# Kernel optimization log

Hardware: AMD Instinct MI355X
Metric: run time of the kernel (lower is better)

Reference implementation:

```python
import jax, jax.numpy as jnp
import numpy as np

N = 50000      # nodes
E = 400000     # edges
F_IN = 128     # num_features
EMB = 64       # embedding_size
H1, H2, H3 = 4, 2, 1
G = 256        # number of graphs in batch
NEG_SLOPE = 0.2  # GATv2Conv default


def setup_inputs() -> dict:
    key = jax.random.key(0)
    ks = jax.random.split(key, 20)
    s = 0.1  # keep attention logits in a sane range
    return {
        "x": jax.random.normal(ks[0], (N, F_IN), dtype=jnp.float32),
        "edge_index": jax.random.randint(ks[1], (2, E), 0, N),
        "batch_index": jnp.sort(jax.random.randint(ks[2], (N,), 0, G)),
        "w1_l": jax.random.normal(ks[3], (H1 * EMB, F_IN), dtype=jnp.float32) * s,
        "w1_r": jax.random.normal(ks[4], (H1 * EMB, F_IN), dtype=jnp.float32) * s,
        "att1": jax.random.normal(ks[5], (H1, EMB), dtype=jnp.float32) * s,
        "b1": jax.random.normal(ks[6], (H1 * EMB,), dtype=jnp.float32) * s,
        "w2_l": jax.random.normal(ks[7], (H2 * EMB, H1 * EMB), dtype=jnp.float32) * s,
        "w2_r": jax.random.normal(ks[8], (H2 * EMB, H1 * EMB), dtype=jnp.float32) * s,
        "att2": jax.random.normal(ks[9], (H2, EMB), dtype=jnp.float32) * s,
        "b2": jax.random.normal(ks[10], (H2 * EMB,), dtype=jnp.float32) * s,
        "w3_l": jax.random.normal(ks[11], (H3 * EMB, H2 * EMB), dtype=jnp.float32) * s,
        "w3_r": jax.random.normal(ks[12], (H3 * EMB, H2 * EMB), dtype=jnp.float32) * s,
        "att3": jax.random.normal(ks[13], (H3, EMB), dtype=jnp.float32) * s,
        "b3": jax.random.normal(ks[14], (H3 * EMB,), dtype=jnp.float32) * s,
        "out_w": jax.random.normal(ks[15], (2, 2 * EMB), dtype=jnp.float32) * s,
        "out_b": jax.random.normal(ks[16], (2,), dtype=jnp.float32) * s,
    }


def gatv2_conv(x, src, dst, w_l, w_r, att, bias, heads):
    """PyG GATv2Conv (concat=True, add_self_loops already applied to src/dst)."""
    n = x.shape[0]
    d = att.shape[1]
    xl = (x @ w_l.T).reshape(n, heads, d)   # source transform
    xr = (x @ w_r.T).reshape(n, heads, d)   # target transform
    # per-edge attention logits: e_ij = att . leaky_relu(xl[j] + xr[i])
    z = jax.nn.leaky_relu(xl[src] + xr[dst], NEG_SLOPE)      # [E', H, D]
    e = jnp.einsum("ehd,hd->eh", z, att)                      # [E', H]
    # segment softmax over incoming edges of each target node
    m = jax.ops.segment_max(e, dst, num_segments=n)           # [N, H]
    p = jnp.exp(e - m[dst])
    ssum = jax.ops.segment_sum(p, dst, num_segments=n)        # [N, H]
    alpha = p / (ssum[dst] + 1e-16)
    out = jax.ops.segment_sum(alpha[:, :, None] * xl[src], dst, num_segments=n)
    return out.reshape(n, heads * d) + bias


def reference(x, edge_index, batch_index,
              w1_l, w1_r, att1, b1,
              w2_l, w2_r, att2, b2,
              w3_l, w3_r, att3, b3,
              out_w, out_b):
    n = x.shape[0]
    loop = jnp.arange(n, dtype=edge_index.dtype)
    src = jnp.concatenate([edge_index[0], loop])  # add self loops (PyG default)
    dst = jnp.concatenate([edge_index[1], loop])

    h = gatv2_conv(x, src, dst, w1_l, w1_r, att1, b1, H1)
    h = jax.nn.leaky_relu(h)  # slope 0.01 (F.leaky_relu default)
    h = gatv2_conv(h, src, dst, w2_l, w2_r, att2, b2, H2)
    h = jax.nn.leaky_relu(h)
    h = gatv2_conv(h, src, dst, w3_l, w3_r, att3, b3, H3)
    h = jax.nn.leaky_relu(h)

    # global max / mean pooling per graph
    gmax = jax.ops.segment_max(h, batch_index, num_segments=G)
    gsum = jax.ops.segment_sum(h, batch_index, num_segments=G)
    cnt = jax.ops.segment_sum(jnp.ones((n, 1), h.dtype), batch_index, num_segments=G)
    gmean = gsum / jnp.maximum(cnt, 1.0)
    hidden = jnp.concatenate([gmax, gmean], axis=1)           # [G, 2*EMB]
    out = hidden @ out_w.T + out_b                            # [G, 2]
    return (out, hidden)
```

## Files before the change

### kernel.cpp

```cpp
#include <hip/hip_runtime.h>
#include <hip/hip_bf16.h>
#include <cfloat>
#include <cstdint>


typedef __attribute__((ext_vector_type(8))) short bf16x8;
typedef __attribute__((ext_vector_type(4))) float f32x4;
typedef __attribute__((ext_vector_type(2))) float v2f;
typedef __attribute__((ext_vector_type(4))) unsigned short us4;
typedef __attribute__((ext_vector_type(2))) unsigned short us2;

#define L2E 1.4426950408889634f

__device__ __forceinline__ float bf2f(unsigned short u) {
    return __uint_as_float((unsigned)u << 16);
}
__device__ __forceinline__ unsigned short f2bf(float f) {
    unsigned u = __float_as_uint(f);
    u += 0x7FFFu + ((u >> 16) & 1u);
    return (unsigned short)(u >> 16);
}
__device__ __forceinline__ v2f unpack2(unsigned d) {
    v2f r;
    r.x = __uint_as_float(d << 16);
    r.y = __uint_as_float(d & 0xffff0000u);
    return r;
}
__device__ __forceinline__ unsigned pack2(float a, float b) {
    return (unsigned)f2bf(a) | ((unsigned)f2bf(b) << 16);
}

template<int CTRL>
__device__ __forceinline__ float dpp_add_f(float x) {
    int xi = __float_as_int(x);
    int yi = __builtin_amdgcn_update_dpp(xi, xi, CTRL, 0xF, 0xF, false);
    return x + __int_as_float(yi);
}
template<int PAT>
__device__ __forceinline__ float swz_add_f(float x) {
    int yi = __builtin_amdgcn_ds_swizzle(__float_as_int(x), PAT);
    return x + __int_as_float(yi);
}
template<int GS>
__device__ __forceinline__ float group_sum(float p) {
    p = dpp_add_f<0x121>(p);
    p = dpp_add_f<0x122>(p);
    p = dpp_add_f<0x124>(p);
    p = dpp_add_f<0x128>(p);
    if constexpr (GS >= 32) p = swz_add_f<0x401F>(p);
    if constexpr (GS >= 64) p += __shfl_xor(p, 32, 64);
    return p;
}

__global__ void init_k(int* __restrict__ deg, float* __restrict__ gsum,
                       float* __restrict__ gcnt, unsigned* __restrict__ gmaxu,
                       int N, int G)
{
    int i = blockIdx.x * blockDim.x + threadIdx.x;
    int stride = gridDim.x * blockDim.x;
    for (int k = i; k < N; k += stride) deg[k] = 0;
    for (int k = i; k < G * 64; k += stride) { gsum[k] = 0.f; gmaxu[k] = 0x00800000u; }
    for (int k = i; k < G; k += stride) gcnt[k] = 0.f;
}

__global__ void prep_k(const float* __restrict__ x, unsigned short* __restrict__ xb, int nx,
                       const float* p0, const float* p1, const float* p2,
                       const float* p3, const float* p4, const float* p5,
                       unsigned short* d0, unsigned short* d1, unsigned short* d2,
                       unsigned short* d3, unsigned short* d4, unsigned short* d5,
                       int s01, int s23, int s45,
                       const int* __restrict__ dste, int E, int N, int* __restrict__ deg)
{
    const int tid = blockIdx.x * blockDim.x + threadIdx.x;
    const int stride = gridDim.x * blockDim.x;

    for (int i = tid; i < nx / 4; i += stride) {
        int idx = i * 4;
        float4 v = *(const float4*)(x + idx);
        uint2 o = { pack2(v.x, v.y), pack2(v.z, v.w) };
        *(uint2*)(xb + idx) = o;
    }
    const int wtot4 = (2 * s01 + 2 * s23 + 2 * s45) / 4;
    const int t0 = 2 * s01, t1 = t0 + 2 * s23;
    for (int i = tid; i < wtot4; i += stride) {
        int e = i * 4;
        const float* s; unsigned short* d; int off;
        if (e < t0)      { int j = e;      s = (j < s01) ? p0 : p1; d = (j < s01) ? d0 : d1; off = j % s01; }
        else if (e < t1) { int j = e - t0; s = (j < s23) ? p2 : p3; d = (j < s23) ? d2 : d3; off = j % s23; }
        else             { int j = e - t1; s = (j < s45) ? p4 : p5; d = (j < s45) ? d4 : d5; off = j % s45; }
        float4 v = *(const float4*)(s + off);
        uint2 o = { pack2(v.x, v.y), pack2(v.z, v.w) };
        *(uint2*)(d + off) = o;
    }
    for (int e = tid; e < E + N; e += stride) {
        int i = (e < E) ? dste[e] : (e - E);
        atomicAdd(&deg[i], 1);
    }
}

template<int NT, int KT>
__global__ __launch_bounds__(256) void gemm_mfma(
    const __hip_bfloat16* __restrict__ A,
    const __hip_bfloat16* __restrict__ Wl, const __hip_bfloat16* __restrict__ Wr,
    __hip_bfloat16* __restrict__ Cl, __hip_bfloat16* __restrict__ Cr,
    int M, int Nout)
{
    constexpr int K = KT * 32;
    constexpr int LSTR = NT * 16 + 8;
    __shared__ unsigned short lds_c[4][32 * LSTR];
    const int wave = threadIdx.x >> 6, lane = threadIdx.x & 63;
    const int m0 = (blockIdx.x * 4 + wave) * 32;
    if (m0 >= M) return;
    const __hip_bfloat16* W = blockIdx.y ? Wr : Wl;
    __hip_bfloat16* C = blockIdx.y ? Cr : Cl;
    const int nbase = blockIdx.z * NT * 16;
    const int r16  = lane & 15;
    const int quad = lane >> 4;
    const int kq = quad * 8;

    f32x4 acc[2][NT];
    #pragma unroll
    for (int mt = 0; mt < 2; ++mt)
        #pragma unroll
        for (int n = 0; n < NT; ++n) acc[mt][n] = (f32x4){0.f, 0.f, 0.f, 0.f};

    const __hip_bfloat16* Arow[2];
    #pragma unroll
    for (int mt = 0; mt < 2; ++mt) {
        int r = m0 + mt * 16 + r16;
        r = (r < M) ? r : (M - 1);
        Arow[mt] = A + (size_t)r * K + kq;
    }
    const __hip_bfloat16* Wbase = W + (size_t)(nbase + r16) * K + kq;

    #pragma unroll
    for (int kt = 0; kt < KT; ++kt) {
        const int k0 = kt * 32;
        bf16x8 a[2];
        #pragma unroll
        for (int mt = 0; mt < 2; ++mt)
            a[mt] = *(const bf16x8*)(Arow[mt] + k0);
        #pragma unroll
        for (int n = 0; n < NT; ++n) {
            bf16x8 b = *(const bf16x8*)(Wbase + (size_t)n * 16 * K + k0);
            #pragma unroll
            for (int mt = 0; mt < 2; ++mt)
                acc[mt][n] = __builtin_amdgcn_mfma_f32_16x16x32_bf16(a[mt], b, acc[mt][n], 0, 0, 0);
        }
    }

    unsigned short* L = &lds_c[wave][0];
    #pragma unroll
    for (int mt = 0; mt < 2; ++mt)
        #pragma unroll
        for (int n = 0; n < NT; ++n)
            #pragma unroll
            for (int r = 0; r < 4; ++r)
                L[(mt * 16 + quad * 4 + r) * LSTR + n * 16 + r16] = f2bf(acc[mt][n][r]);
    constexpr int LPR = NT * 2;
    constexpr int RPI = 64 / LPR;
    const int il = lane % LPR;
    const int rr = lane / LPR;
    unsigned short* Cu = (unsigned short*)C;
    #pragma unroll
    for (int t = 0; t < 32 / RPI; ++t) {
        int row = t * RPI + rr;
        uint4 v = *(const uint4*)(L + row * LSTR + il * 8);
        int grow = m0 + row;
        if (grow < M)
            *(uint4*)(Cu + (size_t)grow * Nout + nbase + il * 8) = v;
    }
}

__global__ __launch_bounds__(1024) void scanA_k(const int* __restrict__ deg,
                                                int* __restrict__ rowptr,
                                                int* __restrict__ bsum, int N)
{
    __shared__ int parts[16];
    const int t = threadIdx.x, lane = t & 63, wv = t >> 6;
    const int base = blockIdx.x * 8192;
    int v[8];
    int run = 0;
    #pragma unroll
    for (int i = 0; i < 8; ++i) {
        int idx = base + t * 8 + i;
        run += (idx < N) ? deg[idx] : 0;
        v[i] = run;
    }
    int x = run;
    #pragma unroll
    for (int off = 1; off < 64; off <<= 1) {
        int y = __shfl_up(x, off, 64);
        if (lane >= off) x += y;
    }
    int excl = x - run;
    if (lane == 63) parts[wv] = x;
    __syncthreads();
    if (wv == 0 && lane < 16) {
        int p = parts[lane];
        int xx = p;
        #pragma unroll
        for (int off = 1; off < 16; off <<= 1) {
            int y = __shfl_up(xx, off, 64);
            if (lane >= off) xx += y;
        }
        parts[lane] = xx - p;
    }
    __syncthreads();
    int pre = parts[wv] + excl;
    #pragma unroll
    for (int i = 0; i < 8; ++i) {
        int idx = base + t * 8 + i;
        if (idx < N) rowptr[idx + 1] = pre + v[i];
    }
    if (t == 1023) bsum[blockIdx.x] = parts[15] + x;
}

__global__ void scanB_k(int* __restrict__ bsum, int B)
{
    int lane = threadIdx.x;
    int v = (lane < B) ? bsum[lane] : 0;
    int x = v;
    #pragma unroll
    for (int off = 1; off < 64; off <<= 1) {
        int y = __shfl_up(x, off, 64);
        if (lane >= off) x += y;
    }
    if (lane < B) bsum[lane] = x - v;
}

__global__ __launch_bounds__(1024) void scanC_k(int* __restrict__ rowptr,
                                                const int* __restrict__ bsum, int N)
{
    const int b = blockIdx.x, t = threadIdx.x;
    if (b == 0) { if (t == 0) rowptr[0] = 0; return; }
    const int off = bsum[b];
    const int base = b * 8192;
    #pragma unroll
    for (int i = 0; i < 8; ++i) {
        int idx = base + t * 8 + i;
        if (idx < N) rowptr[idx + 1] += off;
    }
}

__global__ void scatter_k(const int* __restrict__ src, const int* __restrict__ dst,
                          int E, int N, const int* __restrict__ rowptr,
                          int* __restrict__ deg, int* __restrict__ esrc)
{
    int e = blockIdx.x * blockDim.x + threadIdx.x;
    if (e >= E + N) return;
    int i = (e < E) ? dst[e] : (e - E);
    int j = (e < E) ? src[e] : (e - E);
    int old = atomicAdd(&deg[i], -1);
    esrc[rowptr[i] + old - 1] = j;
}

template<int P>
__device__ __forceinline__ float edge_logit(const v2f* xv, const v2f* xrv, const v2f* attv)
{
    v2f d = {0.f, 0.f};
    #pragma unroll
    for (int p = 0; p < P; ++p) {
        v2f z = xv[p] + xrv[p];
        v2f l = __builtin_elementwise_max(z, z * 0.2f);
        d += l * attv[p];
    }
    return d.x + d.y;
}

template<int P>
__device__ __forceinline__ void load_edge(const unsigned short* __restrict__ xl,
                                          size_t base, v2f* xv)
{
    if constexpr (P == 2) {
        uint2 a = *(const uint2*)(xl + base);
        xv[0] = unpack2(a.x); xv[1] = unpack2(a.y);
    } else {
        unsigned a = *(const unsigned*)(xl + base);
        xv[0] = unpack2(a);
    }
}

template<int H, bool BF16OUT>
__global__ __launch_bounds__(256) void fused_agg_k(
    const unsigned short* __restrict__ xl, const unsigned short* __restrict__ xr,
    const int* __restrict__ rowptr, const int* __restrict__ esrc,
    const float* __restrict__ att, const float* __restrict__ bias,
    void* __restrict__ outv, int N, float oslope)
{
    const int wid  = __builtin_amdgcn_readfirstlane(
                         (blockIdx.x * blockDim.x + threadIdx.x) >> 6);
    const int lane = threadIdx.x & 63;
    if (wid >= N) return;
    constexpr int HD = H * 64;
    constexpr int GS = 64 / H;
    const int f0 = lane * H;
    const int r0 = rowptr[wid];
    const int r1 = rowptr[wid + 1];

    if constexpr (H >= 2) {
        constexpr int P = H / 2;
        v2f xrv[P], attv[P], acc[P];
        load_edge<P>(xr, (size_t)wid * HD + f0, xrv);
        #pragma unroll
        for (int p = 0; p < P; ++p) {
            attv[p] = *(const v2f*)(att + f0 + 2 * p) * L2E;
            acc[p] = (v2f){0.f, 0.f};
        }

        float s = 0.f;
        int k = r0;
        for (; k + 4 <= r1; k += 4) {
            int j[4];
            #pragma unroll
            for (int i = 0; i < 4; ++i) j[i] = esrc[k + i];
            v2f xv[4][P];
            #pragma unroll
            for (int i = 0; i < 4; ++i)
                load_edge<P>(xl, (size_t)j[i] * HD + f0, xv[i]);
            float pl[4];
            #pragma unroll
            for (int i = 0; i < 4; ++i) pl[i] = edge_logit<P>(xv[i], xrv, attv);
            #pragma unroll
            for (int i = 0; i < 4; ++i) pl[i] = group_sum<GS>(pl[i]);
            float w[4];
            #pragma unroll
            for (int i = 0; i < 4; ++i) w[i] = __builtin_amdgcn_exp2f(pl[i]);
            s += (w[0] + w[1]) + (w[2] + w[3]);
            #pragma unroll
            for (int p = 0; p < P; ++p) {
                v2f t = xv[0][p] * w[0] + xv[1][p] * w[1];
                t += xv[2][p] * w[2] + xv[3][p] * w[3];
                acc[p] += t;
            }
        }
        for (; k < r1; ++k) {
            int j0 = esrc[k];
            v2f xv[P];
            load_edge<P>(xl, (size_t)j0 * HD + f0, xv);
            float pl = group_sum<GS>(edge_logit<P>(xv, xrv, attv));
            float w = __builtin_amdgcn_exp2f(pl);
            s += w;
            #pragma unroll
            for (int p = 0; p < P; ++p) acc[p] += xv[p] * w;
        }

        float rs = 1.f / (s + 1e-16f);
        unsigned short o[H];
        float of[H];
        #pragma unroll
        for (int p = 0; p < P; ++p) {
            v2f b2 = *(const v2f*)(bias + f0 + 2 * p);
            v2f v = acc[p] * rs + b2;
            v = __builtin_elementwise_max(v, v * oslope);
            if constexpr (BF16OUT) { o[2 * p] = f2bf(v.x); o[2 * p + 1] = f2bf(v.y); }
            else                   { of[2 * p] = v.x; of[2 * p + 1] = v.y; }
        }
        if constexpr (BF16OUT) {
            unsigned short* ou = (unsigned short*)outv;
            if constexpr (H == 4) *(us4*)(ou + (size_t)wid * HD + f0) = *(us4*)o;
            else                  *(us2*)(ou + (size_t)wid * HD + f0) = *(us2*)o;
        } else {
            float* off_ = (float*)outv;
            #pragma unroll
            for (int i = 0; i < H; ++i) off_[(size_t)wid * HD + f0 + i] = of[i];
        }
    } else {
        float xrv  = bf2f(xr[(size_t)wid * 64 + lane]);
        float attv = att[lane] * L2E;
        float s = 0.f, acc = 0.f;
        int k = r0;
        for (; k + 4 <= r1; k += 4) {
            int j[4];
            #pragma unroll
            for (int i = 0; i < 4; ++i) j[i] = esrc[k + i];
            float xv[4], pl[4], w[4];
            #pragma unroll
            for (int i = 0; i < 4; ++i) xv[i] = bf2f(xl[(size_t)j[i] * 64 + lane]);
            #pragma unroll
            for (int i = 0; i < 4; ++i) {
                float z = xv[i] + xrv;
                pl[i] = fmaxf(z, 0.2f * z) * attv;
            }
            #pragma unroll
            for (int i = 0; i < 4; ++i) pl[i] = group_sum<64>(pl[i]);
            #pragma unroll
            for (int i = 0; i < 4; ++i) w[i] = __builtin_amdgcn_exp2f(pl[i]);
            s += (w[0] + w[1]) + (w[2] + w[3]);
            acc += (xv[0] * w[0] + xv[1] * w[1]) + (xv[2] * w[2] + xv[3] * w[3]);
        }
        for (; k < r1; ++k) {
            float x0 = bf2f(xl[(size_t)esrc[k] * 64 + lane]);
            float z = x0 + xrv;
            float pl = group_sum<64>(fmaxf(z, 0.2f * z) * attv);
            float w = __builtin_amdgcn_exp2f(pl);
            s += w;
            acc += x0 * w;
        }
        float rs = 1.f / (s + 1e-16f);
        float v = acc * rs + bias[lane];
        v = fmaxf(v, oslope * v);
        if constexpr (BF16OUT)
            ((unsigned short*)outv)[(size_t)wid * 64 + lane] = f2bf(v);
        else
            ((float*)outv)[(size_t)wid * 64 + lane] = v;
    }
}

__device__ __forceinline__ unsigned fenc(float f) {
    unsigned u = __float_as_uint(f);
    return (u & 0x80000000u) ? ~u : (u | 0x80000000u);
}
__device__ __forceinline__ float fdec(unsigned u) {
    return __uint_as_float((u & 0x80000000u) ? (u & 0x7fffffffu) : ~u);
}

__global__ __launch_bounds__(256) void pool_k(
    const float* __restrict__ h, const int* __restrict__ batch, int N,
    unsigned* __restrict__ gmaxu, float* __restrict__ gsum, float* __restrict__ gcnt)
{
    const int wid  = (blockIdx.x * blockDim.x + threadIdx.x) >> 6;
    const int lane = threadIdx.x & 63;
    const int n0 = wid * 16;
    if (n0 >= N) return;
    int gcur = batch[n0];
    float vmax = -3.4e38f, vsum = 0.f;
    int cnt = 0;
    #pragma unroll 4
    for (int i = 0; i < 16; ++i) {
        int n = n0 + i;
        if (n >= N) break;
        int g = batch[n];
        if (g != gcur) {
            atomicMax(&gmaxu[gcur * 64 + lane], fenc(vmax));
            atomicAdd(&gsum[gcur * 64 + lane], vsum);
            if (lane == 0) atomicAdd(&gcnt[gcur], (float)cnt);
            gcur = g; vmax = -3.4e38f; vsum = 0.f; cnt = 0;
        }
        float v = h[(size_t)n * 64 + lane];
        vmax = fmaxf(vmax, v);
        vsum += v;
        cnt++;
    }
    atomicMax(&gmaxu[gcur * 64 + lane], fenc(vmax));
    atomicAdd(&gsum[gcur * 64 + lane], vsum);
    if (lane == 0) atomicAdd(&gcnt[gcur], (float)cnt);
}

__global__ __launch_bounds__(128) void final_k(
    const unsigned* __restrict__ gmaxu, const float* __restrict__ gsum,
    const float* __restrict__ gcnt, const float* __restrict__ out_w,
    const float* __restrict__ out_b, float* __restrict__ out,
    float* __restrict__ hid_out)
{
    const int g = blockIdx.x;
    const int t = threadIdx.x;
    __shared__ float hid[128];
    float v;
    if (t < 64) {
        v = fdec(gmaxu[g * 64 + t]);
    } else {
        float c = fmaxf(gcnt[g], 1.f);
        v = gsum[g * 64 + (t - 64)] / c;
    }
    hid[t] = v;
    hid_out[(size_t)g * 128 + t] = v;
    __syncthreads();
    const int w = t >> 6, lane = t & 63;
    float p = hid[lane] * out_w[w * 128 + lane] + hid[lane + 64] * out_w[w * 128 + 64 + lane];
    #pragma unroll
    for (int off = 32; off >= 1; off >>= 1) p += __shfl_xor(p, off, 64);
    if (lane == 0) out[g * 2 + w] = p + out_b[w];
}

extern "C" void kernel_launch(void* const* d_in, const int* in_sizes, int n_in,
                              void* d_out, int out_size, void* d_ws, size_t ws_size,
                              hipStream_t stream)
{
    const float* x    = (const float*)d_in[0];
    const int*   ei   = (const int*)d_in[1];
    const int*   batch= (const int*)d_in[2];
    const float* w1l  = (const float*)d_in[3];
    const float* w1r  = (const float*)d_in[4];
    const float* att1 = (const float*)d_in[5];
    const float* b1   = (const float*)d_in[6];
    const float* w2l  = (const float*)d_in[7];
    const float* w2r  = (const float*)d_in[8];
    const float* att2 = (const float*)d_in[9];
    const float* b2   = (const float*)d_in[10];
    const float* w3l  = (const float*)d_in[11];
    const float* w3r  = (const float*)d_in[12];
    const float* att3 = (const float*)d_in[13];
    const float* b3   = (const float*)d_in[14];
    const float* outw = (const float*)d_in[15];
    const float* outb = (const float*)d_in[16];

    const int N   = in_sizes[2];
    const int E   = in_sizes[1] / 2;
    const int E2  = E + N;
    const int G   = 256;
    const int FIN = in_sizes[0] / N;
    const int* src = ei;
    const int* dst = ei + E;

    char* ws = (char*)d_ws;
    size_t off = 0;
    auto alloc = [&](size_t bytes) -> void* {
        void* p = ws + off;
        off = (off + bytes + 255) & ~(size_t)255;
        return p;
    };
    unsigned short* xlb   = (unsigned short*)alloc((size_t)N * 256 * 2);
    unsigned short* xrb   = (unsigned short*)alloc((size_t)N * 256 * 2);
    unsigned short* xb    = (unsigned short*)alloc((size_t)N * 128 * 2);
    unsigned short* hAb   = (unsigned short*)alloc((size_t)N * 256 * 2);
    unsigned short* hBb   = (unsigned short*)alloc((size_t)N * 128 * 2);
    float*          h3    = (float*)alloc((size_t)N * 64 * 4);
    int*            rowptr= (int*)alloc((size_t)(N + 1) * 4);
    int*            deg   = (int*)alloc((size_t)N * 4);
    int*            esrc  = (int*)alloc((size_t)E2 * 4);
    int*            bsum  = (int*)alloc(64 * 4);
    unsigned*       gmaxu = (unsigned*)alloc((size_t)G * 64 * 4);
    float*          gsum  = (float*)alloc((size_t)G * 64 * 4);
    float*          gcnt  = (float*)alloc((size_t)G * 4);
    unsigned short* w1lb  = (unsigned short*)alloc(256 * 128 * 2);
    unsigned short* w1rb  = (unsigned short*)alloc(256 * 128 * 2);
    unsigned short* w2lb  = (unsigned short*)alloc(128 * 256 * 2);
    unsigned short* w2rb  = (unsigned short*)alloc(128 * 256 * 2);
    unsigned short* w3lb  = (unsigned short*)alloc(64 * 128 * 2);
    unsigned short* w3rb  = (unsigned short*)alloc(64 * 128 * 2);

    init_k<<<(N + 255) / 256, 256, 0, stream>>>(deg, gsum, gcnt, gmaxu, N, G);

    const int s1 = 256 * 128, s2 = 128 * 256, s3 = 64 * 128;
    prep_k<<<1024, 256, 0, stream>>>(x, xb, N * FIN,
        w1l, w1r, w2l, w2r, w3l, w3r, w1lb, w1rb, w2lb, w2rb, w3lb, w3rb,
        s1, s2, s3, dst, E, N, deg);

    const int nblk = (N + 8191) / 8192;
    scanA_k<<<nblk, 1024, 0, stream>>>(deg, rowptr, bsum, N);
    scanB_k<<<1, 64, 0, stream>>>(bsum, nblk);
    scanC_k<<<nblk, 1024, 0, stream>>>(rowptr, bsum, N);
    scatter_k<<<(E2 + 255) / 256, 256, 0, stream>>>(src, dst, E, N, rowptr, deg, esrc);

    const int gx  = (N + 127) / 128;
    const int nwb = (N * 64 + 255) / 256;

    gemm_mfma<4, 4><<<dim3(gx, 2, 4), 256, 0, stream>>>(
        (const __hip_bfloat16*)xb, (const __hip_bfloat16*)w1lb, (const __hip_bfloat16*)w1rb,
        (__hip_bfloat16*)xlb, (__hip_bfloat16*)xrb, N, 256);
    fused_agg_k<4, true><<<nwb, 256, 0, stream>>>(xlb, xrb, rowptr, esrc, att1, b1, hAb, N, 0.01f);

    gemm_mfma<4, 8><<<dim3(gx, 2, 2), 256, 0, stream>>>(
        (const __hip_bfloat16*)hAb, (const __hip_bfloat16*)w2lb, (const __hip_bfloat16*)w2rb,
        (__hip_bfloat16*)xlb, (__hip_bfloat16*)xrb, N, 128);
    fused_agg_k<2, true><<<nwb, 256, 0, stream>>>(xlb, xrb, rowptr, esrc, att2, b2, hBb, N, 0.01f);

    gemm_mfma<4, 4><<<dim3(gx, 2, 1), 256, 0, stream>>>(
        (const __hip_bfloat16*)hBb, (const __hip_bfloat16*)w3lb, (const __hip_bfloat16*)w3rb,
        (__hip_bfloat16*)xlb, (__hip_bfloat16*)xrb, N, 64);
    fused_agg_k<1, false><<<nwb, 256, 0, stream>>>(xlb, xrb, rowptr, esrc, att3, b3, h3, N, 0.01f);

    const int pb = (N / 16 + 3) / 4;
    pool_k<<<pb, 256, 0, stream>>>(h3, batch, N, gmaxu, gsum, gcnt);
    final_k<<<G, 128, 0, stream>>>(gmaxu, gsum, gcnt, outw, outb,
                                   (float*)d_out, (float*)d_out + G * 2);
}
```

Baseline: 367.2 us.

## Stage weight slabs in LDS and compute both projections per A load

Replaces the register-direct MFMA GEMM with a kernel that stages weight slabs into shared memory and shares them across four waves covering a 64-row tile. It also computes the left and right projections in the same block, so each A tile is read from global memory once instead of once per side and per column slice. This is meant to cut redundant global reads of A and W. The cost is extra block barriers and more accumulator registers, which may lower occupancy.

```diff
diff --git a/kernel.cpp b/kernel.cpp
--- a/kernel.cpp
+++ b/kernel.cpp
@@ -98,77 +98,94 @@
     }
 }
 
-template<int NT, int KT>
-__global__ __launch_bounds__(256) void gemm_mfma(
-    const __hip_bfloat16* __restrict__ A,
-    const __hip_bfloat16* __restrict__ Wl, const __hip_bfloat16* __restrict__ Wr,
-    __hip_bfloat16* __restrict__ Cl, __hip_bfloat16* __restrict__ Cr,
+template<int K, int SLAB>
+__global__ __launch_bounds__(256) void gemm_lds(
+    const unsigned short* __restrict__ A,
+    const unsigned short* __restrict__ Wl, const unsigned short* __restrict__ Wr,
+    unsigned short* __restrict__ Cl, unsigned short* __restrict__ Cr,
     int M, int Nout)
 {
-    constexpr int K = KT * 32;
-    constexpr int LSTR = NT * 16 + 8;
-    __shared__ unsigned short lds_c[4][32 * LSTR];
-    const int wave = threadIdx.x >> 6, lane = threadIdx.x & 63;
-    const int m0 = (blockIdx.x * 4 + wave) * 32;
-    if (m0 >= M) return;
-    const __hip_bfloat16* W = blockIdx.y ? Wr : Wl;
-    __hip_bfloat16* C = blockIdx.y ? Cr : Cl;
-    const int nbase = blockIdx.z * NT * 16;
-    const int r16  = lane & 15;
-    const int quad = lane >> 4;
-    const int kq = quad * 8;
-
-    f32x4 acc[2][NT];
-    #pragma unroll
-    for (int mt = 0; mt < 2; ++mt)
-        #pragma unroll
-        for (int n = 0; n < NT; ++n) acc[mt][n] = (f32x4){0.f, 0.f, 0.f, 0.f};
-
-    const __hip_bfloat16* Arow[2];
+    constexpr int KC   = 128;
+    constexpr int WPAD = KC + 8;
+    constexpr int NT   = SLAB / 32;
+    __shared__ unsigned short Ws[SLAB * WPAD];
+
+    const int tid = threadIdx.x, wv = tid >> 6, lane = tid & 63;
+    const int r16 = lane & 15, quad = lane >> 4;
+    const int m0 = blockIdx.x * 64;
+    const int mh = (wv >> 1) * 32;
+    const int nh = (wv & 1) * (SLAB / 2);
+    const int ncol0 = blockIdx.y * SLAB;
+
+    f32x4 acc[2][2][NT] = {};
+
+    const unsigned short* Arow[2];
     #pragma unroll
     for (int mt = 0; mt < 2; ++mt) {
-        int r = m0 + mt * 16 + r16;
+        int r = m0 + mh + mt * 16 + r16;
         r = (r < M) ? r : (M - 1);
-        Arow[mt] = A + (size_t)r * K + kq;
-    }
-    const __hip_bfloat16* Wbase = W + (size_t)(nbase + r16) * K + kq;
-
-    #pragma unroll
-    for (int kt = 0; kt < KT; ++kt) {
-        const int k0 = kt * 32;
-        bf16x8 a[2];
+        Arow[mt] = A + (size_t)r * K + quad * 8;
+    }
+
+    for (int kc = 0; kc < K / KC; ++kc) {
+        const int k0 = kc * KC;
+        bf16x8 a[2][4];
         #pragma unroll
         for (int mt = 0; mt < 2; ++mt)
-            a[mt] = *(const bf16x8*)(Arow[mt] + k0);
-        #pragma unroll
-        for (int n = 0; n < NT; ++n) {
-            bf16x8 b = *(const bf16x8*)(Wbase + (size_t)n * 16 * K + k0);
-            #pragma unroll
-            for (int mt = 0; mt < 2; ++mt)
-                acc[mt][n] = __builtin_amdgcn_mfma_f32_16x16x32_bf16(a[mt], b, acc[mt][n], 0, 0, 0);
-        }
-    }
-
-    unsigned short* L = &lds_c[wave][0];
-    #pragma unroll
-    for (int mt = 0; mt < 2; ++mt)
-        #pragma unroll
-        for (int n = 0; n < NT; ++n)
-            #pragma unroll
-            for (int r = 0; r < 4; ++r)
-                L[(mt * 16 + quad * 4 + r) * LSTR + n * 16 + r16] = f2bf(acc[mt][n][r]);
-    constexpr int LPR = NT * 2;
+            #pragma unroll
+            for (int ks = 0; ks < 4; ++ks)
+                a[mt][ks] = *(const bf16x8*)(Arow[mt] + k0 + ks * 32);
+
+        #pragma unroll
+        for (int side = 0; side < 2; ++side) {
+            const unsigned short* W = side ? Wr : Wl;
+            __syncthreads();
+            #pragma unroll
+            for (int it = 0; it < SLAB * KC / 2048; ++it) {
+                int idx8 = (it * 256 + tid) * 8;
+                int row = idx8 >> 7, col = idx8 & 127;
+                bf16x8 v = *(const bf16x8*)(W + (size_t)(ncol0 + row) * K + k0 + col);
+                *(bf16x8*)(&Ws[row * WPAD + col]) = v;
+            }
+            __syncthreads();
+            #pragma unroll
+            for (int ks = 0; ks < 4; ++ks) {
+                #pragma unroll
+                for (int n = 0; n < NT; ++n) {
+                    bf16x8 b = *(const bf16x8*)(&Ws[(nh + n * 16 + r16) * WPAD + ks * 32 + quad * 8]);
+                    #pragma unroll
+                    for (int mt = 0; mt < 2; ++mt)
+                        acc[side][mt][n] = __builtin_amdgcn_mfma_f32_16x16x32_bf16(
+                            a[mt][ks], b, acc[side][mt][n], 0, 0, 0);
+                }
+            }
+        }
+    }
+
+    constexpr int RP  = SLAB / 2 + 8;
+    constexpr int LPR = SLAB / 16;
     constexpr int RPI = 64 / LPR;
-    const int il = lane % LPR;
-    const int rr = lane / LPR;
-    unsigned short* Cu = (unsigned short*)C;
-    #pragma unroll
-    for (int t = 0; t < 32 / RPI; ++t) {
-        int row = t * RPI + rr;
-        uint4 v = *(const uint4*)(L + row * LSTR + il * 8);
-        int grow = m0 + row;
-        if (grow < M)
-            *(uint4*)(Cu + (size_t)grow * Nout + nbase + il * 8) = v;
+    const int il = lane % LPR, rr = lane / LPR;
+    #pragma unroll
+    for (int side = 0; side < 2; ++side) {
+        unsigned short* C = side ? Cr : Cl;
+        __syncthreads();
+        unsigned short* L = &Ws[wv * 32 * RP];
+        #pragma unroll
+        for (int mt = 0; mt < 2; ++mt)
+            #pragma unroll
+            for (int n = 0; n < NT; ++n)
+                #pragma unroll
+                for (int r = 0; r < 4; ++r)
+                    L[(mt * 16 + quad * 4 + r) * RP + n * 16 + r16] = f2bf(acc[side][mt][n][r]);
+        #pragma unroll
+        for (int t = 0; t < 32 / RPI; ++t) {
+            int row = t * RPI + rr;
+            uint4 v = *(const uint4*)(&L[row * RP + il * 8]);
+            int gr = m0 + mh + row;
+            if (gr < M)
+                *(uint4*)(C + (size_t)gr * Nout + ncol0 + nh + il * 8) = v;
+        }
     }
 }
 
@@ -543,22 +560,19 @@
     scanC_k<<<nblk, 1024, 0, stream>>>(rowptr, bsum, N);
     scatter_k<<<(E2 + 255) / 256, 256, 0, stream>>>(src, dst, E, N, rowptr, deg, esrc);
 
-    const int gx  = (N + 127) / 128;
+    const int gx  = (N + 63) / 64;
     const int nwb = (N * 64 + 255) / 256;
 
-    gemm_mfma<4, 4><<<dim3(gx, 2, 4), 256, 0, stream>>>(
-        (const __hip_bfloat16*)xb, (const __hip_bfloat16*)w1lb, (const __hip_bfloat16*)w1rb,
-        (__hip_bfloat16*)xlb, (__hip_bfloat16*)xrb, N, 256);
+    gemm_lds<128, 128><<<dim3(gx, 2), 256, 0, stream>>>(
+        xb, w1lb, w1rb, xlb, xrb, N, 256);
     fused_agg_k<4, true><<<nwb, 256, 0, stream>>>(xlb, xrb, rowptr, esrc, att1, b1, hAb, N, 0.01f);
 
-    gemm_mfma<4, 8><<<dim3(gx, 2, 2), 256, 0, stream>>>(
-        (const __hip_bfloat16*)hAb, (const __hip_bfloat16*)w2lb, (const __hip_bfloat16*)w2rb,
-        (__hip_bfloat16*)xlb, (__hip_bfloat16*)xrb, N, 128);
+    gemm_lds<256, 128><<<dim3(gx, 1), 256, 0, stream>>>(
+        hAb, w2lb, w2rb, xlb, xrb, N, 128);
     fused_agg_k<2, true><<<nwb, 256, 0, stream>>>(xlb, xrb, rowptr, esrc, att2, b2, hBb, N, 0.01f);
 
-    gemm_mfma<4, 4><<<dim3(gx, 2, 1), 256, 0, stream>>>(
-        (const __hip_bfloat16*)hBb, (const __hip_bfloat16*)w3lb, (const __hip_bfloat16*)w3rb,
-        (__hip_bfloat16*)xlb, (__hip_bfloat16*)xrb, N, 64);
+    gemm_lds<128, 64><<<dim3(gx, 1), 256, 0, stream>>>(
+        hBb, w3lb, w3rb, xlb, xrb, N, 64);
     fused_agg_k<1, false><<<nwb, 256, 0, stream>>>(xlb, xrb, rowptr, esrc, att3, b3, h3, N, 0.01f);
 
     const int pb = (N / 16 + 3) / 4;
```

Result: faster. 332.5 us (-9.4%).
